# Kernel optimization log

Hardware: AMD Instinct MI355X
Metric: run time of the kernel (lower is better)

## Reference

```python
import jax, jax.numpy as jnp
import numpy as np

POOL = 7  # cfg.POOLING_SIZE


def roi_align_avg(feat, rois, scale):
    """Legacy RoIAlignAvg: bilinearly sample a (POOL+1)x(POOL+1) grid per RoI
    (crop_and_resize semantics: grid spans roi with divisor G-1), then 2x2
    average-pool with stride 1 -> POOL x POOL output. feat: [B,C,H,W]."""
    B, C, H, W = feat.shape
    G = POOL + 1
    b = rois[:, 0].astype(jnp.int32)                                  # [R]
    x1 = rois[:, 1] * scale
    y1 = rois[:, 2] * scale
    x2 = rois[:, 3] * scale
    y2 = rois[:, 4] * scale
    t = jnp.arange(G, dtype=feat.dtype) / (G - 1)                     # [G]
    ty = jnp.clip(y1[:, None] + (y2 - y1)[:, None] * t, 0.0, H - 1)   # [R,G] rows
    tx = jnp.clip(x1[:, None] + (x2 - x1)[:, None] * t, 0.0, W - 1)   # [R,G] cols
    y0f, x0f = jnp.floor(ty), jnp.floor(tx)
    wy = (ty - y0f)[:, :, None, None]                                 # row frac
    wx = (tx - x0f)[:, None, :, None]                                 # col frac
    y0 = y0f.astype(jnp.int32)
    x0 = x0f.astype(jnp.int32)
    y1i = jnp.minimum(y0 + 1, H - 1)
    x1i = jnp.minimum(x0 + 1, W - 1)

    def g(yi, xi):  # point gather -> [R,G,G,C]
        return feat[b[:, None, None], :, yi[:, :, None], xi[:, None, :]]

    v = ((1 - wy) * ((1 - wx) * g(y0, x0) + wx * g(y0, x1i))
         + wy * ((1 - wx) * g(y1i, x0) + wx * g(y1i, x1i)))           # [R,G,G,C]
    v = jnp.transpose(v, (0, 3, 1, 2))                                # [R,C,G,G]
    # 2x2 avg pool, stride 1 -> [R,C,POOL,POOL]
    return 0.25 * (v[:, :, :-1, :-1] + v[:, :, 1:, :-1]
                   + v[:, :, :-1, 1:] + v[:, :, 1:, 1:])


def reference(p2, p3, p4, p5, rois, im_info):
    """_PyramidRoI_Feat (POOLING_MODE='align'): data-dependent FPN level
    assignment per RoI, per-level RoIAlignAvg, reassembled in original RoI
    order (equivalent to the concat+sort in the torch code)."""
    h = rois[:, 4] - rois[:, 2] + 1.0
    w = rois[:, 3] - rois[:, 1] + 1.0
    lvl = jnp.floor(jnp.log(jnp.sqrt(h * w) / 224.0) / np.float32(np.log(2.0)) + 4.0)
    lvl = jnp.clip(lvl, 2.0, 5.0)                                     # [R]
    im_h = im_info[0, 0]
    out = 0.0
    for l, feat in zip((2, 3, 4, 5), (p2, p3, p4, p5)):
        scale = feat.shape[2] / im_h
        mask = (lvl == l).astype(feat.dtype)[:, None, None, None]
        out = out + mask * roi_align_avg(feat, rois, scale)
    return out  # [R, C, POOL, POOL]


def setup_inputs() -> dict:
    key = jax.random.key(0)
    ks = jax.random.split(key, 6)
    B, C = 1, 256
    IMH = IMW = 1024.0
    R = 2000
    p2 = jax.random.normal(ks[0], (B, C, 256, 256), jnp.float32)
    p3 = jax.random.normal(ks[1], (B, C, 128, 128), jnp.float32)
    p4 = jax.random.normal(ks[2], (B, C, 64, 64), jnp.float32)
    p5 = jax.random.normal(ks[3], (B, C, 32, 32), jnp.float32)
    # log-uniform box sizes so RoIs spread across all 4 pyramid levels
    wh = jnp.exp(jax.random.uniform(ks[4], (R, 2), jnp.float32,
                                    minval=np.log(16.0), maxval=np.log(600.0)))
    xy = jax.random.uniform(ks[5], (R, 2), jnp.float32) * (jnp.array([IMW, IMH]) - wh)
    rois = jnp.concatenate([
        jnp.zeros((R, 1), jnp.float32),            # batch index
        xy[:, 0:1], xy[:, 1:2],                    # x1, y1
        xy[:, 0:1] + wh[:, 0:1] - 1.0,             # x2
        xy[:, 1:2] + wh[:, 1:2] - 1.0,             # y2
    ], axis=1)
    im_info = jnp.array([[IMH, IMW, 1.0]], jnp.float32)
    return {"p2": p2, "p3": p3, "p4": p4, "p5": p5, "rois": rois, "im_info": im_info}
```

## Files before the change

kernel.cpp:

```cpp
#include <hip/hip_runtime.h>
#include <hip/hip_fp16.h>
#include <math.h>

#define POOLSZ 7
#define GRIDG 8
#define CCH  256
#define NBIN 256
#define OPP  (POOLSZ * POOLSZ)
#define SPAD 51
#define MAXPER 8

__device__ __forceinline__ int roi_level(const float* __restrict__ rois, int r) {
    const float x1 = rois[r * 5 + 1];
    const float y1 = rois[r * 5 + 2];
    const float x2 = rois[r * 5 + 3];
    const float y2 = rois[r * 5 + 4];
    const float h = __fadd_rn(__fsub_rn(y2, y1), 1.0f);
    const float w = __fadd_rn(__fsub_rn(x2, x1), 1.0f);
    const float s = __fsqrt_rn(__fmul_rn(h, w));
    const float LOG2 = __uint_as_float(0x3F317218u);
    float lv = floorf(__fadd_rn(__fdiv_rn(logf(__fdiv_rn(s, 224.0f)), LOG2), 4.0f));
    lv = fminf(fmaxf(lv, 2.0f), 5.0f);
    return (int)lv;
}

__global__ __launch_bounds__(1024) void sort_all_kernel(
    const float* __restrict__ rois, const float* __restrict__ im_info,
    int R, int* __restrict__ sorted)
{
    __shared__ int cnt[NBIN];
    __shared__ int tmp[NBIN];
    const int t = threadIdx.x;
    if (t < NBIN) cnt[t] = 0;
    __syncthreads();

    int myR[MAXPER], myBin[MAXPER], mySlot[MAXPER];
    int m = 0;
    const float ih = im_info[0], iw = im_info[1];
    for (int r = t; r < R && m < MAXPER; r += 1024) {
        const int lvl = roi_level(rois, r);
        const float cx = 0.5f * (rois[r * 5 + 1] + rois[r * 5 + 3]);
        const float cy = 0.5f * (rois[r * 5 + 2] + rois[r * 5 + 4]);
        const int tx = min(7, max(0, (int)(cx * 8.0f / iw)));
        const int ty = min(7, max(0, (int)(cy * 8.0f / ih)));
        const int bin = (lvl - 2) * 64 + ty * 8 + tx;
        myR[m] = r; myBin[m] = bin;
        mySlot[m] = atomicAdd(&cnt[bin], 1);
        ++m;
    }
    __syncthreads();

    const int v = (t < NBIN) ? cnt[t] : 0;
    if (t < NBIN) tmp[t] = v;
    __syncthreads();
    for (int s = 1; s < NBIN; s <<= 1) {
        const int u = (t < NBIN && t >= s) ? tmp[t - s] : 0;
        __syncthreads();
        if (t < NBIN) tmp[t] += u;
        __syncthreads();
    }
    if (t < NBIN) cnt[t] = tmp[t] - v;
    __syncthreads();

    for (int i = 0; i < m; ++i)
        sorted[cnt[myBin[i]] + mySlot[i]] = myR[i];
}

__global__ __launch_bounds__(256) void transpose_all_kernel(
    const float* __restrict__ p2, const float* __restrict__ p3,
    const float* __restrict__ p4, const float* __restrict__ p5,
    __half* __restrict__ t2, __half* __restrict__ t3,
    __half* __restrict__ t4, __half* __restrict__ t5,
    int HW2, int HW3, int HW4, int HW5)
{
    const int n2 = (HW2 / 64) * 4, n3 = (HW3 / 64) * 4, n4 = (HW4 / 64) * 4;
    int bid = blockIdx.x;
    const float* src; __half* dst; int HW;
    if (bid < n2)              { src = p2; dst = t2; HW = HW2; }
    else if ((bid -= n2) < n3) { src = p3; dst = t3; HW = HW3; }
    else if ((bid -= n3) < n4) { src = p4; dst = t4; HW = HW4; }
    else { bid -= n4;            src = p5; dst = t5; HW = HW5; }
    const int ptiles = HW / 64;
    const int pt = bid % ptiles, ct = bid / ptiles;
    const int pbase = pt * 64, cbase = ct * 64;
    const int t = threadIdx.x;

    __shared__ float tile[64][65];

    const int l = t & 15, cr = t >> 4;
#pragma unroll
    for (int p = 0; p < 4; ++p) {
        const int c = p * 16 + cr;
        const float4 v = *(const float4*)(src + (size_t)(cbase + c) * HW + pbase + l * 4);
        tile[c][l * 4 + 0] = v.x;
        tile[c][l * 4 + 1] = v.y;
        tile[c][l * 4 + 2] = v.z;
        tile[c][l * 4 + 3] = v.w;
    }
    __syncthreads();

    const int ch2 = t & 31, pr = t >> 5;
#pragma unroll
    for (int p = 0; p < 8; ++p) {
        const int row = p * 8 + pr;
        const __half2 h = __floats2half2_rn(tile[ch2 * 2][row], tile[ch2 * 2 + 1][row]);
        *(__half2*)(dst + (size_t)(pbase + row) * CCH + cbase + ch2 * 2) = h;
    }
}

__global__ __launch_bounds__(256) void fpn_main_t(
    const __half* __restrict__ t2, const __half* __restrict__ t3,
    const __half* __restrict__ t4, const __half* __restrict__ t5,
    const float* __restrict__ rois, const float* __restrict__ im_info,
    float* __restrict__ out, const int* __restrict__ order,
    int H2, int H3, int H4, int H5, int R)
{
    const int n = blockIdx.x;
    const int q = R / 8, rem = R % 8;
    const int xcd = n % 8, idx = n / 8;
    const int nsw = (xcd < rem ? xcd * (q + 1) : rem * (q + 1) + (xcd - rem) * q) + idx;
    const int r = order ? order[nsw] : nsw;
    const int t = threadIdx.x;

    const float x1 = rois[r * 5 + 1];
    const float y1 = rois[r * 5 + 2];
    const float x2 = rois[r * 5 + 3];
    const float y2 = rois[r * 5 + 4];

    const int lvl = roi_level(rois, r);
    const __half* feat;
    int H;
    switch (lvl) {
        case 2:  feat = t2; H = H2; break;
        case 3:  feat = t3; H = H3; break;
        case 4:  feat = t4; H = H4; break;
        default: feat = t5; H = H5; break;
    }
    const int W = H;

    const float im_h  = im_info[0];
    const float scale = __fdiv_rn((float)H, im_h);
    const float ylo = __fmul_rn(y1, scale), yhi = __fmul_rn(y2, scale);
    const float xlo = __fmul_rn(x1, scale), xhi = __fmul_rn(x2, scale);

    float wy[GRIDG], wx[GRIDG];
    int yoff[GRIDG], dy[GRIDG], xoff[GRIDG], dx[GRIDG];
#pragma unroll
    for (int i = 0; i < GRIDG; ++i) {
        const float tf = __fdiv_rn((float)i, (float)(GRIDG - 1));
        float ty = __fadd_rn(ylo, __fmul_rn(__fsub_rn(yhi, ylo), tf));
        ty = fminf(fmaxf(ty, 0.0f), (float)(H - 1));
        const float y0f = floorf(ty);
        const int   y0  = (int)y0f;
        yoff[i] = y0 * W * CCH;
        dy[i]   = (min(y0 + 1, H - 1) - y0) * W * CCH;
        wy[i]   = __fsub_rn(ty, y0f);

        float tx = __fadd_rn(xlo, __fmul_rn(__fsub_rn(xhi, xlo), tf));
        tx = fminf(fmaxf(tx, 0.0f), (float)(W - 1));
        const float x0f = floorf(tx);
        const int   x0  = (int)x0f;
        xoff[i] = x0 * CCH;
        dx[i]   = (min(x0 + 1, W - 1) - x0) * CCH;
        wx[i]   = __fsub_rn(tx, x0f);
    }

    __shared__ float s_out[CCH * SPAD];

    float rowPrev[GRIDG], rowCur[GRIDG];
#pragma unroll
    for (int gy = 0; gy < GRIDG; ++gy) {
        const __half* base = feat + yoff[gy] + t;
        const int dyg = dy[gy];
        const float wyg = wy[gy];
        const float omy = 1.0f - wyg;
#pragma unroll
        for (int gx = 0; gx < GRIDG; ++gx) {
            const __half* qp = base + xoff[gx];
            const int dxg = dx[gx];
            const float v00 = __half2float(qp[0]);
            const float v01 = __half2float(qp[dxg]);
            const float v10 = __half2float(qp[dyg]);
            const float v11 = __half2float(qp[dyg + dxg]);
            const float wxg = wx[gx];
            const float omx = 1.0f - wxg;
            rowCur[gx] = omy * (omx * v00 + wxg * v01) + wyg * (omx * v10 + wxg * v11);
        }
        if (gy > 0) {
            const int py = gy - 1;
#pragma unroll
            for (int px = 0; px < POOLSZ; ++px) {
                s_out[t * SPAD + py * POOLSZ + px] =
                    0.25f * (rowPrev[px] + rowPrev[px + 1] + rowCur[px] + rowCur[px + 1]);
            }
        }
#pragma unroll
        for (int gx = 0; gx < GRIDG; ++gx) rowPrev[gx] = rowCur[gx];
    }

    __syncthreads();
    float* obase = out + (size_t)r * (CCH * OPP);
#pragma unroll
    for (int i = 0; i < OPP; ++i) {
        const unsigned k = (unsigned)(i * CCH + t);
        const unsigned c = (k * 21400u) >> 20;
        const unsigned pp = k - c * 49u;
        __builtin_nontemporal_store(s_out[c * SPAD + pp], obase + k);
    }
}

__global__ __launch_bounds__(256) void fpn_roialign_kernel(
    const float* __restrict__ p2, const float* __restrict__ p3,
    const float* __restrict__ p4, const float* __restrict__ p5,
    const float* __restrict__ rois, const float* __restrict__ im_info,
    float* __restrict__ out, const int* __restrict__ order,
    int H2, int H3, int H4, int H5, int R)
{
    const int n = blockIdx.x;
    const int q = R / 8, rem = R % 8;
    const int xcd = n % 8, idx = n / 8;
    const int nsw = (xcd < rem ? xcd * (q + 1) : rem * (q + 1) + (xcd - rem) * q) + idx;
    const int r = order ? order[nsw] : nsw;

    const float bf = rois[r * 5 + 0];
    const float x1 = rois[r * 5 + 1];
    const float y1 = rois[r * 5 + 2];
    const float x2 = rois[r * 5 + 3];
    const float y2 = rois[r * 5 + 4];

    const int lvl = roi_level(rois, r);
    const float* feat;
    int H;
    switch (lvl) {
        case 2:  feat = p2; H = H2; break;
        case 3:  feat = p3; H = H3; break;
        case 4:  feat = p4; H = H4; break;
        default: feat = p5; H = H5; break;
    }
    const int W = H;
    const int wv  = threadIdx.x >> 6;
    const int lid = threadIdx.x & 63;
    const int gy  = lid >> 3;
    const int gx  = lid & 7;

    const float im_h  = im_info[0];
    const float scale = __fdiv_rn((float)H, im_h);
    const float ylo = __fmul_rn(y1, scale), yhi = __fmul_rn(y2, scale);
    const float xlo = __fmul_rn(x1, scale), xhi = __fmul_rn(x2, scale);
    float ty = __fadd_rn(ylo, __fmul_rn(__fsub_rn(yhi, ylo),
                                        __fdiv_rn((float)gy, (float)(GRIDG - 1))));
    ty = fminf(fmaxf(ty, 0.0f), (float)(H - 1));
    float tx = __fadd_rn(xlo, __fmul_rn(__fsub_rn(xhi, xlo),
                                        __fdiv_rn((float)gx, (float)(GRIDG - 1))));
    tx = fminf(fmaxf(tx, 0.0f), (float)(W - 1));
    const float y0f = floorf(ty), x0f = floorf(tx);
    const int   y0  = (int)y0f,   x0  = (int)x0f;
    const int   y1i = min(y0 + 1, H - 1);
    const int   x1i = min(x0 + 1, W - 1);
    const float wyv = __fsub_rn(ty, y0f);
    const float wxv = __fsub_rn(tx, x0f);
    const float omy = 1.0f - wyv;
    const float omx = 1.0f - wxv;

    const int b = (int)bf;
    const size_t plane = (size_t)H * W;
    const float* fbase = feat + (size_t)(b * CCH + wv * 64) * plane;
    const int o00 = y0  * W + x0;
    const int o01 = y0  * W + x1i;
    const int o10 = y1i * W + x0;
    const int o11 = y1i * W + x1i;

    float* obase = out + (size_t)r * (CCH * OPP) + (size_t)(wv * 64) * OPP;
    const bool wr  = (gy < POOLSZ) && (gx < POOLSZ);
    const int oidx = gy * POOLSZ + gx;

#pragma unroll 4
    for (int k = 0; k < 64; ++k) {
        const float* f = fbase + (size_t)k * plane;
        const float v00 = f[o00];
        const float v01 = f[o01];
        const float v10 = f[o10];
        const float v11 = f[o11];
        const float v = omy * (omx * v00 + wxv * v01) + wyv * (omx * v10 + wxv * v11);
        const float vb  = __shfl_down(v, 8);
        const float vr  = __shfl_down(v, 1);
        const float vbr = __shfl_down(v, 9);
        if (wr) obase[k * OPP + oidx] = 0.25f * (((v + vb) + vr) + vbr);
    }
}

extern "C" void kernel_launch(void* const* d_in, const int* in_sizes, int n_in,
                              void* d_out, int out_size, void* d_ws, size_t ws_size,
                              hipStream_t stream) {
    const float* p2      = (const float*)d_in[0];
    const float* p3      = (const float*)d_in[1];
    const float* p4      = (const float*)d_in[2];
    const float* p5      = (const float*)d_in[3];
    const float* rois    = (const float*)d_in[4];
    const float* im_info = (const float*)d_in[5];
    float* out = (float*)d_out;

    const int R = in_sizes[4] / 5;
    auto dimOf = [](int sz) {
        int hw = sz / CCH;
        return (int)(sqrtf((float)hw) + 0.5f);
    };
    const int H2 = dimOf(in_sizes[0]);
    const int H3 = dimOf(in_sizes[1]);
    const int H4 = dimOf(in_sizes[2]);
    const int H5 = dimOf(in_sizes[3]);
    const size_t HW2 = (size_t)H2 * H2, HW3 = (size_t)H3 * H3;
    const size_t HW4 = (size_t)H4 * H4, HW5 = (size_t)H5 * H5;

    const size_t sortBytes = (size_t)R * sizeof(int);
    const size_t sortPad   = (sortBytes + 255) & ~(size_t)255;
    const size_t transBytes = (HW2 + HW3 + HW4 + HW5) * CCH * sizeof(__half);
    const bool canSort  = (ws_size >= sortBytes) && (R <= 1024 * MAXPER);
    const bool canTrans = ws_size >= sortPad + transBytes;

    const int* order = nullptr;
    if (canSort) {
        int* sorted = (int*)d_ws;
        sort_all_kernel<<<1, 1024, 0, stream>>>(rois, im_info, R, sorted);
        order = sorted;
    }

    if (canTrans) {
        __half* t2 = (__half*)((char*)d_ws + sortPad);
        __half* t3 = t2 + HW2 * CCH;
        __half* t4 = t3 + HW3 * CCH;
        __half* t5 = t4 + HW4 * CCH;
        const unsigned nblk = (unsigned)((HW2 + HW3 + HW4 + HW5) / 64 * 4);
        transpose_all_kernel<<<nblk, 256, 0, stream>>>(
            p2, p3, p4, p5, t2, t3, t4, t5,
            (int)HW2, (int)HW3, (int)HW4, (int)HW5);
        fpn_main_t<<<R, 256, 0, stream>>>(
            t2, t3, t4, t5, rois, im_info, out, order, H2, H3, H4, H5, R);
    } else {
        fpn_roialign_kernel<<<R, 256, 0, stream>>>(
            p2, p3, p4, p5, rois, im_info, out, order, H2, H3, H4, H5, R);
    }
}
```

Before: 65.95 us.

## Fuse RoI sort into transpose kernel, store fp16 staging, vectorize output stores

The single-block sort kernel becomes an extra block of the transpose kernel, so one launch and its serial dependency are gone. The transpose uses nontemporal vector loads. The main kernel's shared staging buffer switches from fp32 to fp16, which halves LDS use and may raise occupancy, at the cost of extra rounding on the output. Output writes become 4-wide nontemporal stores. With 256 threads the sort now handles at most 2048 RoIs, which still covers R=2000, and the sort block now runs alongside the transpose blocks instead of before them.

```diff
diff --git a/kernel.cpp b/kernel.cpp
--- a/kernel.cpp
+++ b/kernel.cpp
@@ -7,8 +7,10 @@
 #define CCH  256
 #define NBIN 256
 #define OPP  (POOLSZ * POOLSZ)
-#define SPAD 51
+#define SPADH 51
 #define MAXPER 8
+
+typedef float  fx4 __attribute__((ext_vector_type(4)));
 
 __device__ __forceinline__ int roi_level(const float* __restrict__ rois, int r) {
     const float x1 = rois[r * 5 + 1];
@@ -24,55 +26,56 @@
     return (int)lv;
 }
 
-__global__ __launch_bounds__(1024) void sort_all_kernel(
-    const float* __restrict__ rois, const float* __restrict__ im_info,
-    int R, int* __restrict__ sorted)
-{
-    __shared__ int cnt[NBIN];
-    __shared__ int tmp[NBIN];
-    const int t = threadIdx.x;
-    if (t < NBIN) cnt[t] = 0;
-    __syncthreads();
-
-    int myR[MAXPER], myBin[MAXPER], mySlot[MAXPER];
-    int m = 0;
-    const float ih = im_info[0], iw = im_info[1];
-    for (int r = t; r < R && m < MAXPER; r += 1024) {
-        const int lvl = roi_level(rois, r);
-        const float cx = 0.5f * (rois[r * 5 + 1] + rois[r * 5 + 3]);
-        const float cy = 0.5f * (rois[r * 5 + 2] + rois[r * 5 + 4]);
-        const int tx = min(7, max(0, (int)(cx * 8.0f / iw)));
-        const int ty = min(7, max(0, (int)(cy * 8.0f / ih)));
-        const int bin = (lvl - 2) * 64 + ty * 8 + tx;
-        myR[m] = r; myBin[m] = bin;
-        mySlot[m] = atomicAdd(&cnt[bin], 1);
-        ++m;
-    }
-    __syncthreads();
-
-    const int v = (t < NBIN) ? cnt[t] : 0;
-    if (t < NBIN) tmp[t] = v;
-    __syncthreads();
-    for (int s = 1; s < NBIN; s <<= 1) {
-        const int u = (t < NBIN && t >= s) ? tmp[t - s] : 0;
-        __syncthreads();
-        if (t < NBIN) tmp[t] += u;
-        __syncthreads();
-    }
-    if (t < NBIN) cnt[t] = tmp[t] - v;
-    __syncthreads();
-
-    for (int i = 0; i < m; ++i)
-        sorted[cnt[myBin[i]] + mySlot[i]] = myR[i];
-}
-
-__global__ __launch_bounds__(256) void transpose_all_kernel(
+__global__ __launch_bounds__(256) void prep_kernel(
     const float* __restrict__ p2, const float* __restrict__ p3,
     const float* __restrict__ p4, const float* __restrict__ p5,
     __half* __restrict__ t2, __half* __restrict__ t3,
     __half* __restrict__ t4, __half* __restrict__ t5,
-    int HW2, int HW3, int HW4, int HW5)
+    int HW2, int HW3, int HW4, int HW5,
+    const float* __restrict__ rois, const float* __restrict__ im_info,
+    int R, int* __restrict__ sorted, int nblkT)
 {
+    const int t = threadIdx.x;
+
+    if ((int)blockIdx.x == nblkT) {
+        __shared__ int cnt[NBIN];
+        __shared__ int tmp[NBIN];
+        cnt[t] = 0;
+        __syncthreads();
+
+        int myR[MAXPER], myBin[MAXPER], mySlot[MAXPER];
+        int m = 0;
+        const float ih = im_info[0], iw = im_info[1];
+        for (int r = t; r < R && m < MAXPER; r += 256) {
+            const int lvl = roi_level(rois, r);
+            const float cx = 0.5f * (rois[r * 5 + 1] + rois[r * 5 + 3]);
+            const float cy = 0.5f * (rois[r * 5 + 2] + rois[r * 5 + 4]);
+            const int tx = min(7, max(0, (int)(cx * 8.0f / iw)));
+            const int ty = min(7, max(0, (int)(cy * 8.0f / ih)));
+            const int bin = (lvl - 2) * 64 + ty * 8 + tx;
+            myR[m] = r; myBin[m] = bin;
+            mySlot[m] = atomicAdd(&cnt[bin], 1);
+            ++m;
+        }
+        __syncthreads();
+
+        const int v = cnt[t];
+        tmp[t] = v;
+        __syncthreads();
+        for (int s = 1; s < NBIN; s <<= 1) {
+            const int u = (t >= s) ? tmp[t - s] : 0;
+            __syncthreads();
+            tmp[t] += u;
+            __syncthreads();
+        }
+        cnt[t] = tmp[t] - v;
+        __syncthreads();
+
+        for (int i = 0; i < m; ++i)
+            sorted[cnt[myBin[i]] + mySlot[i]] = myR[i];
+        return;
+    }
+
     const int n2 = (HW2 / 64) * 4, n3 = (HW3 / 64) * 4, n4 = (HW4 / 64) * 4;
     int bid = blockIdx.x;
     const float* src; __half* dst; int HW;
@@ -83,7 +86,6 @@
     const int ptiles = HW / 64;
     const int pt = bid % ptiles, ct = bid / ptiles;
     const int pbase = pt * 64, cbase = ct * 64;
-    const int t = threadIdx.x;
 
     __shared__ float tile[64][65];
 
@@ -91,7 +93,8 @@
 #pragma unroll
     for (int p = 0; p < 4; ++p) {
         const int c = p * 16 + cr;
-        const float4 v = *(const float4*)(src + (size_t)(cbase + c) * HW + pbase + l * 4);
+        const fx4* sp = (const fx4*)(src + (size_t)(cbase + c) * HW + pbase + l * 4);
+        const fx4 v = __builtin_nontemporal_load(sp);
         tile[c][l * 4 + 0] = v.x;
         tile[c][l * 4 + 1] = v.y;
         tile[c][l * 4 + 2] = v.z;
@@ -165,7 +168,7 @@
         wx[i]   = __fsub_rn(tx, x0f);
     }
 
-    __shared__ float s_out[CCH * SPAD];
+    __shared__ unsigned short s_out[CCH * SPADH];
 
     float rowPrev[GRIDG], rowCur[GRIDG];
 #pragma unroll
@@ -190,8 +193,10 @@
             const int py = gy - 1;
 #pragma unroll
             for (int px = 0; px < POOLSZ; ++px) {
-                s_out[t * SPAD + py * POOLSZ + px] =
-                    0.25f * (rowPrev[px] + rowPrev[px + 1] + rowCur[px] + rowCur[px + 1]);
+                const float pv = 0.25f * (rowPrev[px] + rowPrev[px + 1]
+                                          + rowCur[px] + rowCur[px + 1]);
+                s_out[t * SPADH + py * POOLSZ + px] =
+                    __half_as_ushort(__float2half_rn(pv));
             }
         }
 #pragma unroll
@@ -200,12 +205,23 @@
 
     __syncthreads();
     float* obase = out + (size_t)r * (CCH * OPP);
-#pragma unroll
-    for (int i = 0; i < OPP; ++i) {
-        const unsigned k = (unsigned)(i * CCH + t);
+    auto rd = [&](unsigned k) -> float {
         const unsigned c = (k * 21400u) >> 20;
         const unsigned pp = k - c * 49u;
-        __builtin_nontemporal_store(s_out[c * SPAD + pp], obase + k);
+        return __half2float(__ushort_as_half(s_out[c * SPADH + pp]));
+    };
+#pragma unroll
+    for (int i = 0; i < 12; ++i) {
+        const unsigned k4 = (unsigned)(i * 256 + t) * 4u;
+        fx4 v;
+        v.x = rd(k4 + 0); v.y = rd(k4 + 1); v.z = rd(k4 + 2); v.w = rd(k4 + 3);
+        __builtin_nontemporal_store(v, (fx4*)(obase + k4));
+    }
+    if (t < 64) {
+        const unsigned k4 = (unsigned)(12 * 256 + t) * 4u;
+        fx4 v;
+        v.x = rd(k4 + 0); v.y = rd(k4 + 1); v.z = rd(k4 + 2); v.w = rd(k4 + 3);
+        __builtin_nontemporal_store(v, (fx4*)(obase + k4));
     }
 }
 
@@ -315,29 +331,25 @@
     const size_t sortBytes = (size_t)R * sizeof(int);
     const size_t sortPad   = (sortBytes + 255) & ~(size_t)255;
     const size_t transBytes = (HW2 + HW3 + HW4 + HW5) * CCH * sizeof(__half);
-    const bool canSort  = (ws_size >= sortBytes) && (R <= 1024 * MAXPER);
+    const bool canSort  = (ws_size >= sortBytes) && (R <= 256 * MAXPER);
     const bool canTrans = ws_size >= sortPad + transBytes;
 
-    const int* order = nullptr;
-    if (canSort) {
-        int* sorted = (int*)d_ws;
-        sort_all_kernel<<<1, 1024, 0, stream>>>(rois, im_info, R, sorted);
-        order = sorted;
-    }
-
     if (canTrans) {
+        int* sorted = canSort ? (int*)d_ws : nullptr;
         __half* t2 = (__half*)((char*)d_ws + sortPad);
         __half* t3 = t2 + HW2 * CCH;
         __half* t4 = t3 + HW3 * CCH;
         __half* t5 = t4 + HW4 * CCH;
-        const unsigned nblk = (unsigned)((HW2 + HW3 + HW4 + HW5) / 64 * 4);
-        transpose_all_kernel<<<nblk, 256, 0, stream>>>(
+        const int nblkT = (int)((HW2 + HW3 + HW4 + HW5) / 64 * 4);
+        const int nblk  = nblkT + (canSort ? 1 : 0);
+        prep_kernel<<<nblk, 256, 0, stream>>>(
             p2, p3, p4, p5, t2, t3, t4, t5,
-            (int)HW2, (int)HW3, (int)HW4, (int)HW5);
+            (int)HW2, (int)HW3, (int)HW4, (int)HW5,
+            rois, im_info, R, sorted, nblkT);
         fpn_main_t<<<R, 256, 0, stream>>>(
-            t2, t3, t4, t5, rois, im_info, out, order, H2, H3, H4, H5, R);
+            t2, t3, t4, t5, rois, im_info, out, sorted, H2, H3, H4, H5, R);
     } else {
         fpn_roialign_kernel<<<R, 256, 0, stream>>>(
-            p2, p3, p4, p5, rois, im_info, out, order, H2, H3, H4, H5, R);
-    }
-}
+            p2, p3, p4, p5, rois, im_info, out, nullptr, H2, H3, H4, H5, R);
+    }
+}
```

Result: slower. 69.32 us (+5.1%).
